# Kernel optimization log

Measured on AMD Instinct MI355X. Metric: run time of the kernel, lower is better.

The kernel has to match this reference:

```python
import jax, jax.numpy as jnp
import numpy as np

B, S, D = 4, 4096, 1024

def setup_inputs() -> dict:
    key = jax.random.key(0)
    k1, k2, k3 = jax.random.split(key, 3)
    x = jax.random.normal(k1, (B, S, D), dtype=jnp.float32)
    # learned scalar decay logit; original initializes to 0.9 then sigmoids it
    decay_param = jnp.float32(0.9)
    # gate weight [D, D]; original inits to zeros (identity module) -- use small
    # random values so the baseline exercises the full math path
    W_gate = jax.random.normal(k3, (D, D), dtype=jnp.float32) * 0.02
    return {"x": x, "decay_param": decay_param, "W_gate": W_gate}

def reference(x, decay_param, W_gate):
    # x: [B, S, D]
    d = jax.nn.sigmoid(decay_param)  # scalar

    def step(state, x_t):
        # state, x_t: [B, D]
        new = d * state + (1.0 - d) * x_t
        return new, new

    x_t_first = jnp.swapaxes(x, 0, 1)  # [S, B, D]
    init = jnp.zeros((x.shape[0], x.shape[2]), dtype=x.dtype)
    _, causal = jax.lax.scan(step, init, x_t_first)  # [S, B, D]
    causal = jnp.swapaxes(causal, 0, 1)  # [B, S, D]
    # nn.Linear(D, D, bias=False): y = causal @ W^T
    return x + jnp.einsum('bsd,ed->bse', causal, W_gate)
```

## Files before the change

kernel.cpp:

```cpp
#include <hip/hip_runtime.h>
#include <hip/hip_bf16.h>

#define B_DIM 4
#define S_DIM 4096
#define D_DIM 1024
#define M_TOT (B_DIM * S_DIM)
#define LOOKBACK 32
#define CHUNK 128
#define NT (D_DIM / 64)

typedef unsigned short us;
typedef __attribute__((ext_vector_type(8))) short bf16x8;
typedef __attribute__((ext_vector_type(4))) float f32x4;
typedef __attribute__((ext_vector_type(4))) unsigned short u16x4;

__device__ __forceinline__ us f2bf(float f) {
  unsigned int u = __builtin_bit_cast(unsigned int, f);
  u += 0x7fffu + ((u >> 16) & 1u);
  return (us)(u >> 16);
}

__global__ __launch_bounds__(256) void scan_kernel(
    const float* __restrict__ x, const float* __restrict__ dp,
    us* __restrict__ causal) {
  const float dcy = 1.0f / (1.0f + expf(-dp[0]));
  const float omd = 1.0f - dcy;
  const int d0 = blockIdx.x * 512 + threadIdx.x;
  const int s0 = blockIdx.y * CHUNK;
  const size_t base = (size_t)blockIdx.z * S_DIM * D_DIM + d0;
  float st0 = 0.f, st1 = 0.f;
  if (s0 > 0) {
    const float* px = x + base + (size_t)(s0 - LOOKBACK) * D_DIM;
#pragma unroll 8
    for (int i = 0; i < LOOKBACK; ++i) {
      st0 = dcy * st0 + omd * px[0];
      st1 = dcy * st1 + omd * px[256];
      px += D_DIM;
    }
  }
  const float* px = x + base + (size_t)s0 * D_DIM;
  us* pc = causal + base + (size_t)s0 * D_DIM;
#pragma unroll 8
  for (int i = 0; i < CHUNK; ++i) {
    st0 = dcy * st0 + omd * px[0];
    st1 = dcy * st1 + omd * px[256];
    pc[0]   = f2bf(st0);
    pc[256] = f2bf(st1);
    px += D_DIM;
    pc += D_DIM;
  }
}

__global__ __launch_bounds__(256) void convw_kernel(
    const float* __restrict__ W, us* __restrict__ Wb) {
  const int i = (blockIdx.x * 256 + threadIdx.x) * 4;
  const float4 v = *(const float4*)(W + i);
  u16x4 o;
  o.x = f2bf(v.x); o.y = f2bf(v.y); o.z = f2bf(v.z); o.w = f2bf(v.w);
  *(u16x4*)(Wb + i) = o;
}

__global__ __launch_bounds__(256, 3) void gemm_kernel(
    const us* __restrict__ A,
    const us* __restrict__ Bw,
    const float* __restrict__ x,
    float* __restrict__ out) {
  __shared__ us smem_s[24576];

  const int bid = blockIdx.x;
  const int xcd = bid & 7;
  const int q = bid >> 3;
  const int m0 = (xcd * 16 + (q >> 3)) * 128;
  const int n0 = (q & 7) * 128;

  const int tid = threadIdx.x;
  const int lane = tid & 63;
  const int wave = tid >> 6;
  const int wr = wave >> 1;
  const int wc = wave & 1;
  const int lrow = lane & 15;
  const int ls   = lane >> 4;
  const int koff0 = ((0 + ls) ^ (lane & 7)) * 8;
  const int koff1 = ((4 + ls) ^ (lane & 7)) * 8;
  const int arow = (wr * 64 + lrow) * 64;
  const int brow = (wc * 64 + lrow) * 64;

  f32x4 acc[4][4];
#pragma unroll
  for (int i = 0; i < 4; ++i)
#pragma unroll
    for (int j = 0; j < 4; ++j) acc[i][j] = (f32x4)0.f;

#define STAGE(SRC, rowbase, t, ldsbase)                                        \
  {                                                                            \
    _Pragma("unroll")                                                          \
    for (int it = 0; it < 4; ++it) {                                           \
      const int c = it * 256 + tid;                               \
      const int r = c >> 3;                                       \
      const int slot = (c & 7) ^ (r & 7);                                      \
      __builtin_amdgcn_global_load_lds(                                        \
          (const __attribute__((address_space(1))) void*)((SRC) +              \
              (size_t)((rowbase) + r) * D_DIM + (t) * 64 + slot * 8),          \
          (__attribute__((address_space(3))) void*)(smem_s + (ldsbase) + c * 8),\
          16, 0, 0);                                                           \
    }                                                                          \
  }

  STAGE(A,  m0, 0, 0);
  STAGE(Bw, n0, 0, 16384);
  asm volatile("s_waitcnt vmcnt(0)" ::: "memory");
  __builtin_amdgcn_s_barrier();

  for (int t = 0; t < NT; ++t) {
    const int p = t & 1;
    const us* Ab = smem_s + p * 8192;
    const us* Bb = smem_s + 16384;

    bf16x8 b[4][2], a0[4], a1[4];
#pragma unroll
    for (int nj = 0; nj < 4; ++nj) {
      b[nj][0] = *(const bf16x8*)(Bb + brow + nj * 1024 + koff0);
      b[nj][1] = *(const bf16x8*)(Bb + brow + nj * 1024 + koff1);
    }
#pragma unroll
    for (int mi = 0; mi < 4; ++mi)
      a0[mi] = *(const bf16x8*)(Ab + arow + mi * 1024 + koff0);

    __builtin_amdgcn_s_barrier();

    if (t + 1 < NT) {
      STAGE(Bw, n0, t + 1, 16384);
      STAGE(A,  m0, t + 1, (p ^ 1) * 8192);
    }

#pragma unroll
    for (int mi = 0; mi < 4; ++mi)
      a1[mi] = *(const bf16x8*)(Ab + arow + mi * 1024 + koff1);

    __builtin_amdgcn_s_setprio(1);
#pragma unroll
    for (int mi = 0; mi < 4; ++mi)
#pragma unroll
      for (int nj = 0; nj < 4; ++nj)
        acc[mi][nj] = __builtin_amdgcn_mfma_f32_16x16x32_bf16(
            a0[mi], b[nj][0], acc[mi][nj], 0, 0, 0);
#pragma unroll
    for (int mi = 0; mi < 4; ++mi)
#pragma unroll
      for (int nj = 0; nj < 4; ++nj)
        acc[mi][nj] = __builtin_amdgcn_mfma_f32_16x16x32_bf16(
            a1[mi], b[nj][1], acc[mi][nj], 0, 0, 0);
    __builtin_amdgcn_s_setprio(0);

    asm volatile("s_waitcnt vmcnt(0)" ::: "memory");
    __builtin_amdgcn_s_barrier();
  }

#pragma unroll
  for (int mi = 0; mi < 4; ++mi)
#pragma unroll
    for (int nj = 0; nj < 4; ++nj) {
      const int ocol = n0 + wc * 64 + nj * 16 + lrow;
      const int orow0 = m0 + wr * 64 + mi * 16 + ls * 4;
#pragma unroll
      for (int r = 0; r < 4; ++r) {
        const size_t idx = (size_t)(orow0 + r) * D_DIM + ocol;
        out[idx] = x[idx] + acc[mi][nj][r];
      }
    }
#undef STAGE
}

extern "C" void kernel_launch(void* const* d_in, const int* in_sizes, int n_in,
                              void* d_out, int out_size, void* d_ws, size_t ws_size,
                              hipStream_t stream) {
  const float* x  = (const float*)d_in[0];
  const float* dp = (const float*)d_in[1];
  const float* W  = (const float*)d_in[2];
  float* out = (float*)d_out;

  us* causal = (us*)d_ws;
  us* Wb = (us*)((char*)d_ws + (size_t)M_TOT * D_DIM * 2);

  dim3 g_scan(D_DIM / 512, S_DIM / CHUNK, B_DIM);
  scan_kernel<<<g_scan, 256, 0, stream>>>(x, dp, causal);

  convw_kernel<<<(D_DIM * D_DIM) / (256 * 4), 256, 0, stream>>>(W, Wb);

  gemm_kernel<<<(M_TOT / 128) * (D_DIM / 128), 256, 0, stream>>>(
      causal, Wb, x, out);
}
```

Baseline: 70.20 us.

## Widen GEMM tile to 128x256 with split B staging per half

Widens the GEMM output tile from 128x128 to 128x256, so each A tile in LDS is reused across twice as many output columns. The grid is halved and each wave holds a 64x128 accumulator. The B tile is single-buffered, and its reload is split so the next B half streams in while the second MFMA batch runs. This trades higher register and LDS use (occupancy hint drops from 3 to 2) for less A traffic and fewer blocks.

```diff
diff --git a/kernel.cpp b/kernel.cpp
--- a/kernel.cpp
+++ b/kernel.cpp
@@ -60,18 +60,18 @@
   *(u16x4*)(Wb + i) = o;
 }
 
-__global__ __launch_bounds__(256, 3) void gemm_kernel(
+__global__ __launch_bounds__(256, 2) void gemm_kernel(
     const us* __restrict__ A,
     const us* __restrict__ Bw,
     const float* __restrict__ x,
     float* __restrict__ out) {
-  __shared__ us smem_s[24576];
+  __shared__ us smem_s[32768];
 
   const int bid = blockIdx.x;
   const int xcd = bid & 7;
   const int q = bid >> 3;
-  const int m0 = (xcd * 16 + (q >> 3)) * 128;
-  const int n0 = (q & 7) * 128;
+  const int m0 = (xcd * 16 + (q >> 2)) * 128;
+  const int n0 = (q & 3) * 256;
 
   const int tid = threadIdx.x;
   const int lane = tid & 63;
@@ -83,15 +83,17 @@
   const int koff0 = ((0 + ls) ^ (lane & 7)) * 8;
   const int koff1 = ((4 + ls) ^ (lane & 7)) * 8;
   const int arow = (wr * 64 + lrow) * 64;
-  const int brow = (wc * 64 + lrow) * 64;
-
-  f32x4 acc[4][4];
-#pragma unroll
-  for (int i = 0; i < 4; ++i)
-#pragma unroll
-    for (int j = 0; j < 4; ++j) acc[i][j] = (f32x4)0.f;
-
-#define STAGE(SRC, rowbase, t, ldsbase)                                        \
+  const int brow = (wc * 128 + lrow) * 64;
+
+  f32x4 acc[2][4][4];
+#pragma unroll
+  for (int s = 0; s < 2; ++s)
+#pragma unroll
+    for (int i = 0; i < 4; ++i)
+#pragma unroll
+      for (int j = 0; j < 4; ++j) acc[s][i][j] = (f32x4)0.f;
+
+#define STAGE_A(t, p)                                                          \
   {                                                                            \
     _Pragma("unroll")                                                          \
     for (int it = 0; it < 4; ++it) {                                           \
@@ -99,15 +101,29 @@
       const int r = c >> 3;                                       \
       const int slot = (c & 7) ^ (r & 7);                                      \
       __builtin_amdgcn_global_load_lds(                                        \
-          (const __attribute__((address_space(1))) void*)((SRC) +              \
-              (size_t)((rowbase) + r) * D_DIM + (t) * 64 + slot * 8),          \
-          (__attribute__((address_space(3))) void*)(smem_s + (ldsbase) + c * 8),\
+          (const __attribute__((address_space(1))) void*)(A +                  \
+              (size_t)(m0 + r) * D_DIM + (t) * 64 + slot * 8),                 \
+          (__attribute__((address_space(3))) void*)(smem_s + (p) * 8192 + c * 8),\
           16, 0, 0);                                                           \
     }                                                                          \
   }
-
-  STAGE(A,  m0, 0, 0);
-  STAGE(Bw, n0, 0, 16384);
+#define STAGE_B(t)                                                             \
+  {                                                                            \
+    _Pragma("unroll")                                                          \
+    for (int it = 0; it < 8; ++it) {                                           \
+      const int c = it * 256 + tid;                               \
+      const int r = c >> 3;                                       \
+      const int slot = (c & 7) ^ (r & 7);                                      \
+      __builtin_amdgcn_global_load_lds(                                        \
+          (const __attribute__((address_space(1))) void*)(Bw +                 \
+              (size_t)(n0 + r) * D_DIM + (t) * 64 + slot * 8),                 \
+          (__attribute__((address_space(3))) void*)(smem_s + 16384 + c * 8),   \
+          16, 0, 0);                                                           \
+    }                                                                          \
+  }
+
+  STAGE_A(0, 0);
+  STAGE_B(0);
   asm volatile("s_waitcnt vmcnt(0)" ::: "memory");
   __builtin_amdgcn_s_barrier();
 
@@ -116,40 +132,49 @@
     const us* Ab = smem_s + p * 8192;
     const us* Bb = smem_s + 16384;
 
-    bf16x8 b[4][2], a0[4], a1[4];
+    bf16x8 a[4][2], b[4][2];
+#pragma unroll
+    for (int mi = 0; mi < 4; ++mi) {
+      a[mi][0] = *(const bf16x8*)(Ab + arow + mi * 1024 + koff0);
+      a[mi][1] = *(const bf16x8*)(Ab + arow + mi * 1024 + koff1);
+    }
 #pragma unroll
     for (int nj = 0; nj < 4; ++nj) {
       b[nj][0] = *(const bf16x8*)(Bb + brow + nj * 1024 + koff0);
       b[nj][1] = *(const bf16x8*)(Bb + brow + nj * 1024 + koff1);
     }
-#pragma unroll
-    for (int mi = 0; mi < 4; ++mi)
-      a0[mi] = *(const bf16x8*)(Ab + arow + mi * 1024 + koff0);
-
+    if (t + 1 < NT) STAGE_A(t + 1, p ^ 1);
+
+    __builtin_amdgcn_s_setprio(1);
+#pragma unroll
+    for (int ks = 0; ks < 2; ++ks)
+#pragma unroll
+      for (int mi = 0; mi < 4; ++mi)
+#pragma unroll
+        for (int nj = 0; nj < 4; ++nj)
+          acc[0][mi][nj] = __builtin_amdgcn_mfma_f32_16x16x32_bf16(
+              a[mi][ks], b[nj][ks], acc[0][mi][nj], 0, 0, 0);
+    __builtin_amdgcn_s_setprio(0);
+
+#pragma unroll
+    for (int nj = 0; nj < 4; ++nj) {
+      b[nj][0] = *(const bf16x8*)(Bb + brow + 4096 + nj * 1024 + koff0);
+      b[nj][1] = *(const bf16x8*)(Bb + brow + 4096 + nj * 1024 + koff1);
+    }
+    asm volatile("s_waitcnt lgkmcnt(0)" ::: "memory");
     __builtin_amdgcn_s_barrier();
 
-    if (t + 1 < NT) {
-      STAGE(Bw, n0, t + 1, 16384);
-      STAGE(A,  m0, t + 1, (p ^ 1) * 8192);
-    }
-
-#pragma unroll
-    for (int mi = 0; mi < 4; ++mi)
-      a1[mi] = *(const bf16x8*)(Ab + arow + mi * 1024 + koff1);
+    if (t + 1 < NT) STAGE_B(t + 1);
 
     __builtin_amdgcn_s_setprio(1);
 #pragma unroll
-    for (int mi = 0; mi < 4; ++mi)
-#pragma unroll
-      for (int nj = 0; nj < 4; ++nj)
-        acc[mi][nj] = __builtin_amdgcn_mfma_f32_16x16x32_bf16(
-            a0[mi], b[nj][0], acc[mi][nj], 0, 0, 0);
-#pragma unroll
-    for (int mi = 0; mi < 4; ++mi)
-#pragma unroll
-      for (int nj = 0; nj < 4; ++nj)
-        acc[mi][nj] = __builtin_amdgcn_mfma_f32_16x16x32_bf16(
-            a1[mi], b[nj][1], acc[mi][nj], 0, 0, 0);
+    for (int ks = 0; ks < 2; ++ks)
+#pragma unroll
+      for (int mi = 0; mi < 4; ++mi)
+#pragma unroll
+        for (int nj = 0; nj < 4; ++nj)
+          acc[1][mi][nj] = __builtin_amdgcn_mfma_f32_16x16x32_bf16(
+              a[mi][ks], b[nj][ks], acc[1][mi][nj], 0, 0, 0);
     __builtin_amdgcn_s_setprio(0);
 
     asm volatile("s_waitcnt vmcnt(0)" ::: "memory");
@@ -157,18 +182,21 @@
   }
 
 #pragma unroll
-  for (int mi = 0; mi < 4; ++mi)
-#pragma unroll
-    for (int nj = 0; nj < 4; ++nj) {
-      const int ocol = n0 + wc * 64 + nj * 16 + lrow;
-      const int orow0 = m0 + wr * 64 + mi * 16 + ls * 4;
-#pragma unroll
-      for (int r = 0; r < 4; ++r) {
-        const size_t idx = (size_t)(orow0 + r) * D_DIM + ocol;
-        out[idx] = x[idx] + acc[mi][nj][r];
+  for (int ns = 0; ns < 2; ++ns)
+#pragma unroll
+    for (int mi = 0; mi < 4; ++mi)
+#pragma unroll
+      for (int nj = 0; nj < 4; ++nj) {
+        const int ocol = n0 + wc * 128 + ns * 64 + nj * 16 + lrow;
+        const int orow0 = m0 + wr * 64 + mi * 16 + ls * 4;
+#pragma unroll
+        for (int r = 0; r < 4; ++r) {
+          const size_t idx = (size_t)(orow0 + r) * D_DIM + ocol;
+          out[idx] = x[idx] + acc[ns][mi][nj][r];
+        }
       }
-    }
-#undef STAGE
+#undef STAGE_A
+#undef STAGE_B
 }
 
 extern "C" void kernel_launch(void* const* d_in, const int* in_sizes, int n_in,
@@ -187,6 +215,6 @@
 
   convw_kernel<<<(D_DIM * D_DIM) / (256 * 4), 256, 0, stream>>>(W, Wb);
 
-  gemm_kernel<<<(M_TOT / 128) * (D_DIM / 128), 256, 0, stream>>>(
+  gemm_kernel<<<(M_TOT / 128) * (D_DIM / 256), 256, 0, stream>>>(
       causal, Wb, x, out);
 }
```

New measurement: 67.63 us. 3.7% less time.
